# Kernel tuning notes

Hardware: AMD Instinct MI355X
Metric: run time of the kernel (lower is better)

Reference implementation:

```python
import jax, jax.numpy as jnp
import numpy as np

D_MODEL = 1024
NHEAD = 16
D_K = D_MODEL // NHEAD
B, S = 4, 2048
LN_EPS = 1e-5


def setup_inputs() -> dict:
    key = jax.random.key(0)
    ks = jax.random.split(key, 12)
    sd = 1.0 / np.sqrt(D_MODEL)
    inp = {
        'x': jax.random.normal(ks[0], (B, S, D_MODEL), dtype=jnp.float32),
        'wq': jax.random.normal(ks[1], (D_MODEL, D_MODEL), dtype=jnp.float32) * sd,
        'bq': jnp.zeros((D_MODEL,), dtype=jnp.float32),
        'wk': jax.random.normal(ks[2], (D_MODEL, D_MODEL), dtype=jnp.float32) * sd,
        'bk': jnp.zeros((D_MODEL,), dtype=jnp.float32),
        'wv': jax.random.normal(ks[3], (D_MODEL, D_MODEL), dtype=jnp.float32) * sd,
        'bv': jnp.zeros((D_MODEL,), dtype=jnp.float32),
        'wo': jax.random.normal(ks[4], (D_MODEL, D_MODEL), dtype=jnp.float32) * sd,
        'bo': jnp.zeros((D_MODEL,), dtype=jnp.float32),
        'conv_w': jax.random.normal(ks[5], (D_MODEL, 3), dtype=jnp.float32) * (1.0 / np.sqrt(3.0)),
        'conv_b': jnp.zeros((D_MODEL,), dtype=jnp.float32),
        'ln_g': jnp.ones((D_MODEL,), dtype=jnp.float32),
        'ln_b': jnp.zeros((D_MODEL,), dtype=jnp.float32),
    }
    return inp


def _forward(x, wq, bq, wk, bk, wv, bv, wo, bo, conv_w, conv_b, ln_g, ln_b):
    b, s, d = x.shape
    # QKV projections -> [B, H, S, Dk]
    q = (x @ wq.T + bq).reshape(b, s, NHEAD, D_K).transpose(0, 2, 1, 3)
    k = (x @ wk.T + bk).reshape(b, s, NHEAD, D_K).transpose(0, 2, 1, 3)
    v = (x @ wv.T + bv).reshape(b, s, NHEAD, D_K).transpose(0, 2, 1, 3)
    # full attention, materialized scores [B, H, S, S]
    scores = jnp.einsum('bhqd,bhkd->bhqk', q, k) / jnp.sqrt(jnp.float32(D_K))
    attn = jax.nn.softmax(scores, axis=-1)  # dropout is identity in eval
    ctx = jnp.einsum('bhqk,bhkd->bhqd', attn, v)
    ctx = ctx.transpose(0, 2, 1, 3).reshape(b, s, d)
    global_attn = ctx @ wo.T + bo
    # depthwise conv1d, kernel 3, padding 1 along sequence
    xp = jnp.pad(x, ((0, 0), (1, 1), (0, 0)))
    local_attn = (xp[:, :-2] * conv_w[:, 0]
                  + xp[:, 1:-1] * conv_w[:, 1]
                  + xp[:, 2:] * conv_w[:, 2]
                  + conv_b)
    combined = global_attn + 0.3 * local_attn
    y = x + combined  # dropout identity in eval
    mu = jnp.mean(y, axis=-1, keepdims=True)
    var = jnp.mean(jnp.square(y - mu), axis=-1, keepdims=True)
    return (y - mu) * jax.lax.rsqrt(var + LN_EPS) * ln_g + ln_b


def reference(x, wq, bq, wk, bk, wv, bv, wo, bo, conv_w, conv_b, ln_g, ln_b):
    return _forward(x, wq, bq, wk, bk, wv, bv, wo, bo, conv_w, conv_b, ln_g, ln_b)
```

## Files before the change

kernel.cpp:

```cpp
#include <hip/hip_runtime.h>

#define DEV __device__ __forceinline__

typedef unsigned short u16;
typedef unsigned int u32;
using f32x4  = __attribute__((ext_vector_type(4))) float;
using f32x16 = __attribute__((ext_vector_type(16))) float;
using s16x8  = __attribute__((ext_vector_type(8))) short;
using u32x2  = __attribute__((ext_vector_type(2))) u32;
using u32x4  = __attribute__((ext_vector_type(4))) u32;
typedef int i32x2 __attribute__((ext_vector_type(2)));

#if __has_builtin(__builtin_amdgcn_exp2f)
#define EXP2(x) __builtin_amdgcn_exp2f(x)
#else
#define EXP2(x) exp2f(x)
#endif

__constant__ const float C2_SCALE = 0.18033688011112042f;
#define S2_SHIFT 17.312340490667560f

DEV u16 f2b(float f) {
  union { float f; u32 u; } v; v.f = f;
  return (u16)((v.u + 0x7FFFu + ((v.u >> 16) & 1u)) >> 16);
}
DEV float b2f(u16 u) {
  union { u32 u; float f; } v; v.u = ((u32)u) << 16;
  return v.f;
}

DEV u32 cvtpk(float lo, float hi) {
  u32 r;
  asm("v_cvt_pk_bf16_f32 %0, %1, %2" : "=v"(r) : "v"(lo), "v"(hi));
  return r;
}

#if __has_builtin(__builtin_amdgcn_permlane32_swap)
DEV void lane32_swap(u32& x, u32& y) {
  i32x2 r = __builtin_amdgcn_permlane32_swap((int)x, (int)y, false, false);
  x = (u32)r[0]; y = (u32)r[1];
}
#else
DEV void lane32_swap(u32& x, u32& y) {
  u32 xo = (u32)__shfl_xor((int)x, 32, 64);
  u32 yo = (u32)__shfl_xor((int)y, 32, 64);
  int hi = (int)((threadIdx.x & 63) >> 5);
  u32 nx = hi ? yo : x;
  u32 ny = hi ? y : xo;
  x = nx; y = ny;
}
#endif

DEV void gload16(const void* g, void* l) {
  __builtin_amdgcn_global_load_lds(
      (const __attribute__((address_space(1))) void*)g,
      (__attribute__((address_space(3))) void*)l, 16, 0, 0);
}

__global__ __launch_bounds__(256) void k_cvt(const float* __restrict__ src,
                                             u16* __restrict__ dst, int n4) {
  int i = blockIdx.x * 256 + threadIdx.x;
  if (i >= n4) return;
  float4 v = ((const float4*)src)[i];
  ushort4 o;
  o.x = f2b(v.x); o.y = f2b(v.y); o.z = f2b(v.z); o.w = f2b(v.w);
  ((ushort4*)dst)[i] = o;
}

template <int MODE>
__global__ __launch_bounds__(256) void k_gemm_bt(
    const u16* __restrict__ A, const u16* __restrict__ Bw,
    const float* __restrict__ bias0, const float* __restrict__ bias1,
    u16* __restrict__ C, int M, int N, int K) {
  __shared__ alignas(16) u16 lds_[16384];
  char* lds = (char*)lds_;
  const int t = threadIdx.x;
  const int wave = t >> 6, lane = t & 63;
  const int g = lane >> 4, fr = lane & 15;
  const int wr = (wave >> 1) * 64, wc = (wave & 1) * 64;
  const int m0 = blockIdx.y * 128, n0 = blockIdx.x * 128;
  const int chunk = t & 3;

  auto stage = [&](int k0, int buf) {
#pragma unroll
    for (int r = 0; r < 2; ++r) {
      int row = r * 64 + (t >> 2);
      int sw = 8 * (chunk ^ ((row >> 1) & 3));
      char* dst = lds + buf * 16384 + r * 4096 + wave * 1024;
      gload16(A  + (size_t)(m0 + row) * K + k0 + sw, dst);
      gload16(Bw + (size_t)(n0 + row) * K + k0 + sw, dst + 8192);
    }
  };

  f32x4 acc[4][4];
#pragma unroll
  for (int i = 0; i < 4; ++i)
#pragma unroll
    for (int j = 0; j < 4; ++j)
#pragma unroll
      for (int r = 0; r < 4; ++r) acc[i][j][r] = 0.f;

  const int nk = K >> 5;
  stage(0, 0);
  __syncthreads();
  for (int kt = 0; kt < nk; ++kt) {
    const int cur = kt & 1;
    if (kt + 1 < nk) stage((kt + 1) << 5, cur ^ 1);
    s16x8 af[4], bf4[4];
#pragma unroll
    for (int i = 0; i < 4; ++i) {
      int row = wr + i * 16 + fr;
      af[i] = *(const s16x8*)(lds + cur * 16384 + row * 64 +
                              ((g * 16) ^ ((((row >> 1) & 3)) << 4)));
    }
#pragma unroll
    for (int j = 0; j < 4; ++j) {
      int row = wc + j * 16 + fr;
      bf4[j] = *(const s16x8*)(lds + cur * 16384 + 8192 + row * 64 +
                               ((g * 16) ^ ((((row >> 1) & 3)) << 4)));
    }
    __builtin_amdgcn_s_setprio(1);
#pragma unroll
    for (int i = 0; i < 4; ++i)
#pragma unroll
      for (int j = 0; j < 4; ++j)
        acc[i][j] = __builtin_amdgcn_mfma_f32_16x16x32_bf16(af[i], bf4[j], acc[i][j], 0, 0, 0);
    __builtin_amdgcn_s_setprio(0);
    __syncthreads();
  }
#pragma unroll
  for (int j = 0; j < 4; ++j) {
    const int coltile = n0 + wc + j * 16;
    float sc = 1.f;
    const float* bp = bias0;
    if constexpr (MODE == 2) {
      if (coltile >= 1024) { bp = bias1 - 1024; sc = C2_SCALE; }
    }
#pragma unroll
    for (int i = 0; i < 4; ++i)
#pragma unroll
      for (int r = 0; r < 4; ++r) {
        int row = m0 + wr + i * 16 + g * 4 + r;
        int col = coltile + fr;
        float v;
        if constexpr (MODE == 1) v = acc[i][j][r] + bias0[row];
        else                     v = (acc[i][j][r] + bp[col]) * sc;
        C[(size_t)row * N + col] = f2b(v);
      }
  }
}

__global__ __launch_bounds__(256) void k_attn(
    const u16* __restrict__ qkb, const u16* __restrict__ vtb,
    u16* __restrict__ ctx) {
  __shared__ alignas(16) u16 smem_[16384];
  char* smem = (char*)smem_;
  const int bh = blockIdx.x;
  const int b = bh >> 4, h = bh & 15;
  const int qblk = blockIdx.y;
  const int t = threadIdx.x, w = t >> 6, lane = t & 63;
  const int l31 = lane & 31, hi = lane >> 5;
  const int hc = h * 64;
  const int q0 = qblk * 128 + w * 32;
  const int lrow = lane >> 3, seg = lane & 7;

  s16x8 qf[4];
  {
    const u16* qrow = qkb + (size_t)(b * 2048 + q0 + l31) * 2048 + hc + hi * 8;
#pragma unroll
    for (int ks = 0; ks < 4; ++ks) qf[ks] = *(const s16x8*)(qrow + ks * 16);
  }

  const u16* kbase  = qkb + (size_t)(b * 2048) * 2048 + 1024 + hc;
  const u16* vtbase = vtb + (size_t)hc * 8192 + b * 2048;

  auto stage = [&](int kt, int buf) {
    const int k0 = kt * 64;
#pragma unroll
    for (int r = 0; r < 2; ++r) {
      int row = r * 32 + w * 8 + lrow;
      int sw = 8 * (seg ^ (row & 7));
      char* dst = smem + buf * 16384 + r * 4096 + w * 1024;
      gload16(kbase  + (size_t)(k0 + row) * 2048 + sw, dst);
      gload16(vtbase + (size_t)row * 8192 + k0 + sw, dst + 8192);
    }
  };

  f32x16 octx[2], lacc, ns2;
#pragma unroll
  for (int r = 0; r < 16; ++r) {
    octx[0][r] = 0.f; octx[1][r] = 0.f; lacc[r] = 0.f; ns2[r] = -S2_SHIFT;
  }
  s16x8 ones;
#pragma unroll
  for (int j = 0; j < 8; ++j) ones[j] = (short)0x3F80;

  stage(0, 0);
  __syncthreads();
  for (int kt = 0; kt < 32; ++kt) {
    const int cur = kt & 1;
    if (kt + 1 < 32) stage(kt + 1, cur ^ 1);

    f32x16 st[2];
    __builtin_amdgcn_s_setprio(1);
#pragma unroll
    for (int ks = 0; ks < 4; ++ks)
#pragma unroll
      for (int tt = 0; tt < 2; ++tt) {
        int row = tt * 32 + l31;
        s16x8 kf = *(const s16x8*)(smem + cur * 16384 + row * 128 +
                                   ((ks * 32 + hi * 16) ^ ((row & 7) << 4)));
        st[tt] = __builtin_amdgcn_mfma_f32_32x32x16_bf16(
            kf, qf[ks], ks == 0 ? ns2 : st[tt], 0, 0, 0);
      }
    __builtin_amdgcn_s_setprio(0);

    u32 pw[2][8];
#pragma unroll
    for (int tt = 0; tt < 2; ++tt)
#pragma unroll
      for (int p = 0; p < 8; ++p)
        pw[tt][p] = cvtpk(EXP2(st[tt][2 * p]), EXP2(st[tt][2 * p + 1]));

    s16x8 pf[4];
#pragma unroll
    for (int ks = 0; ks < 4; ++ks) {
      int tt = ks >> 1, kp = (ks & 1) * 4;
      u32 u0 = pw[tt][kp + 0], v0 = pw[tt][kp + 2];
      u32 u1 = pw[tt][kp + 1], v1 = pw[tt][kp + 3];
      lane32_swap(u0, v0);
      lane32_swap(u1, v1);
      u32x4 f; f[0] = u0; f[1] = u1; f[2] = v0; f[3] = v1;
      pf[ks] = __builtin_bit_cast(s16x8, f);
    }

    __builtin_amdgcn_s_setprio(1);
#pragma unroll
    for (int dt = 0; dt < 2; ++dt)
#pragma unroll
      for (int ks = 0; ks < 4; ++ks) {
        int row = dt * 32 + l31;
        s16x8 vf = *(const s16x8*)(smem + cur * 16384 + 8192 + row * 128 +
                                   ((ks * 32 + hi * 16) ^ ((row & 7) << 4)));
        octx[dt] = __builtin_amdgcn_mfma_f32_32x32x16_bf16(vf, pf[ks], octx[dt], 0, 0, 0);
      }
#pragma unroll
    for (int ks = 0; ks < 4; ++ks)
      lacc = __builtin_amdgcn_mfma_f32_32x32x16_bf16(ones, pf[ks], lacc, 0, 0, 0);
    __builtin_amdgcn_s_setprio(0);
    __syncthreads();
  }

  const float linv = 1.0f / lacc[0];

  const int ql = w * 32 + l31;
#pragma unroll
  for (int dt = 0; dt < 2; ++dt)
#pragma unroll
    for (int rq = 0; rq < 4; ++rq) {
      int d0 = 8 * rq + 4 * hi + 32 * dt;
      u32x2 pk;
      pk[0] = cvtpk(octx[dt][4 * rq + 0] * linv, octx[dt][4 * rq + 1] * linv);
      pk[1] = cvtpk(octx[dt][4 * rq + 2] * linv, octx[dt][4 * rq + 3] * linv);
      *(u32x2*)(smem + ql * 128 + ((2 * d0) ^ ((ql & 7) << 4))) = pk;
    }
  __syncthreads();
  {
    int qr = t >> 1, half = t & 1;
    u16* dst = ctx + (size_t)(b * 2048 + qblk * 128 + qr) * 1024 + hc + half * 32;
#pragma unroll
    for (int i = 0; i < 4; ++i) {
      s16x8 v = *(const s16x8*)(smem + qr * 128 +
                                ((half * 64 + i * 16) ^ ((qr & 7) << 4)));
      *(s16x8*)(dst + i * 8) = v;
    }
  }
}

__global__ __launch_bounds__(256) void k_epi(
    const float* __restrict__ x, const u16* __restrict__ gab,
    const float* __restrict__ cw, const float* __restrict__ cb,
    const float* __restrict__ lg, const float* __restrict__ lb,
    float* __restrict__ out) {
  __shared__ float red[4];
  const int n = blockIdx.x;
  const int s = n & 2047;
  const int t = threadIdx.x;
  const int d0 = t * 4;
  const float* xr = x + (size_t)n * 1024;

  float xc[4], xm[4], xp[4];
  { float4 v = *(const float4*)(xr + d0); xc[0]=v.x; xc[1]=v.y; xc[2]=v.z; xc[3]=v.w; }
  if (s > 0) { float4 v = *(const float4*)(xr - 1024 + d0); xm[0]=v.x; xm[1]=v.y; xm[2]=v.z; xm[3]=v.w; }
  else { xm[0]=xm[1]=xm[2]=xm[3]=0.f; }
  if (s < 2047) { float4 v = *(const float4*)(xr + 1024 + d0); xp[0]=v.x; xp[1]=v.y; xp[2]=v.z; xp[3]=v.w; }
  else { xp[0]=xp[1]=xp[2]=xp[3]=0.f; }
  ushort4 gv = *(const ushort4*)(gab + (size_t)n * 1024 + d0);
  float ga4[4] = { b2f(gv.x), b2f(gv.y), b2f(gv.z), b2f(gv.w) };

  float y[4];
#pragma unroll
  for (int i = 0; i < 4; ++i) {
    int d = d0 + i;
    float lo = xm[i] * cw[d * 3] + xc[i] * cw[d * 3 + 1] + xp[i] * cw[d * 3 + 2] + cb[d];
    y[i] = xc[i] + ga4[i] + 0.3f * lo;
  }

  float sm = y[0] + y[1] + y[2] + y[3];
#pragma unroll
  for (int off = 32; off >= 1; off >>= 1) sm += __shfl_xor(sm, off, 64);
  if ((t & 63) == 0) red[t >> 6] = sm;
  __syncthreads();
  float mu = (red[0] + red[1] + red[2] + red[3]) * (1.f / 1024.f);
  __syncthreads();

  float vs = 0.f;
#pragma unroll
  for (int i = 0; i < 4; ++i) { float dd = y[i] - mu; vs += dd * dd; }
#pragma unroll
  for (int off = 32; off >= 1; off >>= 1) vs += __shfl_xor(vs, off, 64);
  if ((t & 63) == 0) red[t >> 6] = vs;
  __syncthreads();
  float var = (red[0] + red[1] + red[2] + red[3]) * (1.f / 1024.f);
  float rs = rsqrtf(var + 1e-5f);
#pragma unroll
  for (int i = 0; i < 4; ++i) {
    int d = d0 + i;
    out[(size_t)n * 1024 + d] = (y[i] - mu) * rs * lg[d] + lb[d];
  }
}

extern "C" void kernel_launch(void* const* d_in, const int* in_sizes, int n_in,
                              void* d_out, int out_size, void* d_ws, size_t ws_size,
                              hipStream_t stream) {
  const float* x  = (const float*)d_in[0];
  const float* wq = (const float*)d_in[1];
  const float* bq = (const float*)d_in[2];
  const float* wk = (const float*)d_in[3];
  const float* bk = (const float*)d_in[4];
  const float* wv = (const float*)d_in[5];
  const float* bv = (const float*)d_in[6];
  const float* wo = (const float*)d_in[7];
  const float* bo = (const float*)d_in[8];
  const float* cw = (const float*)d_in[9];
  const float* cb = (const float*)d_in[10];
  const float* lg = (const float*)d_in[11];
  const float* lb = (const float*)d_in[12];
  float* out = (float*)d_out;

  char* ws = (char*)d_ws;
  const size_t MB = 1ull << 20;
  u16* xb  = (u16*)(ws + 0);
  u16* wqb = (u16*)(ws + 16 * MB);
  u16* wkb = (u16*)(ws + 18 * MB);
  u16* wvb = (u16*)(ws + 20 * MB);
  u16* wob = (u16*)(ws + 22 * MB);
  u16* qkb = (u16*)(ws + 24 * MB);
  u16* vtb = (u16*)(ws + 56 * MB);
  u16* ctx = xb;
  u16* gab = qkb;

  k_cvt<<<8192, 256, 0, stream>>>(x, xb, 2097152);
  k_cvt<<<1024, 256, 0, stream>>>(wq, wqb, 262144);
  k_cvt<<<1024, 256, 0, stream>>>(wk, wkb, 262144);
  k_cvt<<<1024, 256, 0, stream>>>(wv, wvb, 262144);
  k_cvt<<<1024, 256, 0, stream>>>(wo, wob, 262144);

  k_gemm_bt<2><<<dim3(16, 64), 256, 0, stream>>>(xb, wqb, bq, bk, qkb, 8192, 2048, 1024);
  k_gemm_bt<1><<<dim3(64, 8), 256, 0, stream>>>(wvb, xb, bv, nullptr, vtb, 1024, 8192, 1024);

  k_attn<<<dim3(64, 16), 256, 0, stream>>>(qkb, vtb, ctx);

  k_gemm_bt<0><<<dim3(8, 64), 256, 0, stream>>>(ctx, wob, bo, nullptr, gab, 8192, 1024, 1024);

  k_epi<<<8192, 256, 0, stream>>>(x, gab, cw, cb, lg, lb, out);
}
```

Baseline: 223.9 us.

## Double attention query tile per block and fuse weight conversions into one launch

The attention kernel now runs 512 threads (8 waves) per block, and each block covers 256 queries instead of 128. Every staged K/V tile is therefore shared by twice as many query rows, which halves global K/V traffic per query, and each thread issues one async load per tile instead of two. The four separate weight fp32-to-bf16 conversion launches are merged into a single launch to cut launch overhead. The tighter launch bounds of (512, 4) may limit registers per thread and risk spills, and there are fewer blocks to balance across CUs.

```diff
diff --git a/kernel.cpp b/kernel.cpp
--- a/kernel.cpp
+++ b/kernel.cpp
@@ -65,6 +65,20 @@
   ushort4 o;
   o.x = f2b(v.x); o.y = f2b(v.y); o.z = f2b(v.z); o.w = f2b(v.w);
   ((ushort4*)dst)[i] = o;
+}
+
+__global__ __launch_bounds__(256) void k_cvt_w(
+    const float* __restrict__ s0, const float* __restrict__ s1,
+    const float* __restrict__ s2, const float* __restrict__ s3,
+    u16* __restrict__ dst) {
+  int blk = blockIdx.x;
+  int widx = blk >> 10;
+  int i = (blk & 1023) * 256 + threadIdx.x;
+  const float* src = widx == 0 ? s0 : widx == 1 ? s1 : widx == 2 ? s2 : s3;
+  float4 v = ((const float4*)src)[i];
+  ushort4 o;
+  o.x = f2b(v.x); o.y = f2b(v.y); o.z = f2b(v.z); o.w = f2b(v.w);
+  ((ushort4*)(dst + (size_t)widx * 1048576))[i] = o;
 }
 
 template <int MODE>
@@ -150,7 +164,7 @@
   }
 }
 
-__global__ __launch_bounds__(256) void k_attn(
+__global__ __launch_bounds__(512, 4) void k_attn(
     const u16* __restrict__ qkb, const u16* __restrict__ vtb,
     u16* __restrict__ ctx) {
   __shared__ alignas(16) u16 smem_[16384];
@@ -161,8 +175,7 @@
   const int t = threadIdx.x, w = t >> 6, lane = t & 63;
   const int l31 = lane & 31, hi = lane >> 5;
   const int hc = h * 64;
-  const int q0 = qblk * 128 + w * 32;
-  const int lrow = lane >> 3, seg = lane & 7;
+  const int q0 = qblk * 256 + w * 32;
 
   s16x8 qf[4];
   {
@@ -174,16 +187,13 @@
   const u16* kbase  = qkb + (size_t)(b * 2048) * 2048 + 1024 + hc;
   const u16* vtbase = vtb + (size_t)hc * 8192 + b * 2048;
 
+  const int srow = t >> 3, sseg = t & 7;
+  const int ssw = 8 * (sseg ^ (srow & 7));
   auto stage = [&](int kt, int buf) {
     const int k0 = kt * 64;
-#pragma unroll
-    for (int r = 0; r < 2; ++r) {
-      int row = r * 32 + w * 8 + lrow;
-      int sw = 8 * (seg ^ (row & 7));
-      char* dst = smem + buf * 16384 + r * 4096 + w * 1024;
-      gload16(kbase  + (size_t)(k0 + row) * 2048 + sw, dst);
-      gload16(vtbase + (size_t)row * 8192 + k0 + sw, dst + 8192);
-    }
+    char* dst = smem + buf * 16384 + w * 1024;
+    gload16(kbase  + (size_t)(k0 + srow) * 2048 + ssw, dst);
+    gload16(vtbase + (size_t)srow * 8192 + k0 + ssw, dst + 8192);
   };
 
   f32x16 octx[2], lacc, ns2;
@@ -267,7 +277,7 @@
   __syncthreads();
   {
     int qr = t >> 1, half = t & 1;
-    u16* dst = ctx + (size_t)(b * 2048 + qblk * 128 + qr) * 1024 + hc + half * 32;
+    u16* dst = ctx + (size_t)(b * 2048 + qblk * 256 + qr) * 1024 + hc + half * 32;
 #pragma unroll
     for (int i = 0; i < 4; ++i) {
       s16x8 v = *(const s16x8*)(smem + qr * 128 +
@@ -361,15 +371,12 @@
   u16* gab = qkb;
 
   k_cvt<<<8192, 256, 0, stream>>>(x, xb, 2097152);
-  k_cvt<<<1024, 256, 0, stream>>>(wq, wqb, 262144);
-  k_cvt<<<1024, 256, 0, stream>>>(wk, wkb, 262144);
-  k_cvt<<<1024, 256, 0, stream>>>(wv, wvb, 262144);
-  k_cvt<<<1024, 256, 0, stream>>>(wo, wob, 262144);
+  k_cvt_w<<<4096, 256, 0, stream>>>(wq, wk, wv, wo, wqb);
 
   k_gemm_bt<2><<<dim3(16, 64), 256, 0, stream>>>(xb, wqb, bq, bk, qkb, 8192, 2048, 1024);
   k_gemm_bt<1><<<dim3(64, 8), 256, 0, stream>>>(wvb, xb, bv, nullptr, vtb, 1024, 8192, 1024);
 
-  k_attn<<<dim3(64, 16), 256, 0, stream>>>(qkb, vtb, ctx);
+  k_attn<<<dim3(64, 8), 512, 0, stream>>>(qkb, vtb, ctx);
 
   k_gemm_bt<0><<<dim3(8, 64), 256, 0, stream>>>(ctx, wob, bo, nullptr, gab, 8192, 1024, 1024);
 
```

Result: faster. 219.0 us (-2.2%).
